# Performance work log

Measured on AMD Instinct MI355X. Metric: run time of the kernel, lower is better.

The kernel has to match this reference:

```python
import jax, jax.numpy as jnp
import numpy as np

LN_EPS = 1e-5


def setup_inputs() -> dict:
    key = jax.random.key(0)
    k1, k2, k3, k4, k5 = jax.random.split(key, 5)
    V, D_REAL, D_HID, D_MODEL = 32000, 768, 512, 4096
    B, S = 4, 2048
    return {
        "real": jax.random.normal(k1, (V, D_REAL), dtype=jnp.float32),
        "llama_embed": jax.random.normal(k2, (V, D_MODEL), dtype=jnp.float32),
        "w1": jax.random.normal(k3, (D_HID, D_REAL), dtype=jnp.float32),  # trans_1.weight
        "w2": jax.random.normal(k4, (D_MODEL, D_HID), dtype=jnp.float32),  # trans_2.weight
        "ln_w": jnp.ones((D_HID,), dtype=jnp.float32),
        "ln_b": jnp.zeros((D_HID,), dtype=jnp.float32),
        "input_ids": jax.random.randint(k5, (B, S), 0, V, dtype=jnp.int64),
    }


def _layernorm(x, w, b):
    mu = jnp.mean(x, axis=-1, keepdims=True)
    var = jnp.mean(jnp.square(x - mu), axis=-1, keepdims=True)
    return (x - mu) * jax.lax.rsqrt(var + LN_EPS) * w + b


def reference(real, llama_embed, w1, w2, ln_w, ln_b, input_ids):
    # trans_2(ELU(LayerNorm(trans_1(real)))) over the FULL table, as in the original
    h = jnp.einsum("vd,hd->vh", real, w1)            # [V, 512]
    h = jax.nn.elu(_layernorm(h, ln_w, ln_b))        # [V, 512]
    transfered = jnp.einsum("vh,mh->vm", h, w2)      # [V, 4096]
    # gather rows per token and add frozen llama embeddings
    return transfered[input_ids] + llama_embed[input_ids]  # [B, S, 4096]
```

## Files before the change

kernel.cpp:

```cpp
#include <hip/hip_runtime.h>
#include <hip/hip_bf16.h>
#include <math.h>

#define TOKENS 8192
#define D_REAL 768
#define D_HID  512
#define D_MODEL 4096

typedef __attribute__((ext_vector_type(8))) short bf16x8;
typedef __attribute__((ext_vector_type(4))) float f32x4;

__device__ inline unsigned short f2bf(float f) {
    union { float f; unsigned u; } v; v.f = f;
    unsigned r = v.u + 0x7FFFu + ((v.u >> 16) & 1u);
    return (unsigned short)(r >> 16);
}
__device__ inline float bf2f(unsigned short h) {
    union { unsigned u; float f; } v; v.u = ((unsigned)h) << 16;
    return v.f;
}

__device__ inline void gload_lds16(const void* g, void* lds_wave_base) {
    __builtin_amdgcn_global_load_lds(
        (const __attribute__((address_space(1))) unsigned*)g,
        (__attribute__((address_space(3))) unsigned*)lds_wave_base,
        16, 0, 0);
}

template<int K, int N, bool ADD_EMBED, bool OUT_BF16>
__global__ __launch_bounds__(256)
void gemm_mfma(const unsigned short* __restrict__ A,
               const unsigned short* __restrict__ B,
               const int* __restrict__ ids,
               const float* __restrict__ embed,
               void* __restrict__ Cout)
{
    __shared__ __align__(16) unsigned short As[128 * 32];
    __shared__ __align__(16) unsigned short Bs[128 * 32];
    __shared__ int sIds[128];

    const int tid = threadIdx.x;
    const int rowBase = blockIdx.x * 128;
    const int colBase = blockIdx.y * 128;

    if (ADD_EMBED && tid < 128) sIds[tid] = ids[rowBase + tid];

    const int srow = tid >> 2;
    const int scol = (tid & 3) * 8;
    const unsigned short* gA = A + (size_t)(rowBase + srow) * K + scol;
    const unsigned short* gB = B + (size_t)(colBase + srow) * K + scol;
    unsigned short* lA = As + (tid >> 6) * 512;
    unsigned short* lB = Bs + (tid >> 6) * 512;

    const int lane = tid & 63;
    const int wv   = tid >> 6;
    const int wm   = (wv >> 1) * 64;
    const int wn   = (wv & 1) * 64;
    const int frow = lane & 15;
    const int fk   = (lane >> 4) * 8;

    f32x4 acc[4][4];
    #pragma unroll
    for (int i = 0; i < 4; i++)
        #pragma unroll
        for (int j = 0; j < 4; j++) acc[i][j] = (f32x4)0.f;

    for (int k0 = 0; k0 < K; k0 += 32) {
        gload_lds16(gA,                lA);
        gload_lds16(gA + (size_t)64*K, lA + 2048);
        gload_lds16(gB,                lB);
        gload_lds16(gB + (size_t)64*K, lB + 2048);
        gA += 32; gB += 32;
        __syncthreads();

        bf16x8 af[4], bg[4];
        #pragma unroll
        for (int i = 0; i < 4; i++)
            af[i] = *reinterpret_cast<const bf16x8*>(&As[(wm + i*16 + frow) * 32 + fk]);
        #pragma unroll
        for (int j = 0; j < 4; j++)
            bg[j] = *reinterpret_cast<const bf16x8*>(&Bs[(wn + j*16 + frow) * 32 + fk]);

        #pragma unroll
        for (int i = 0; i < 4; i++)
            #pragma unroll
            for (int j = 0; j < 4; j++)
                acc[i][j] = __builtin_amdgcn_mfma_f32_16x16x32_bf16(af[i], bg[j], acc[i][j], 0, 0, 0);
        __syncthreads();
    }

    const int orow0 = wm + (lane >> 4) * 4;
    const int ocol0 = wn + frow;
    #pragma unroll
    for (int i = 0; i < 4; i++) {
        #pragma unroll
        for (int r = 0; r < 4; r++) {
            const int lrow = orow0 + i * 16 + r;
            const size_t grow = (size_t)(rowBase + lrow);
            if (OUT_BF16) {
                unsigned short* C = (unsigned short*)Cout;
                #pragma unroll
                for (int j = 0; j < 4; j++)
                    C[grow * N + colBase + ocol0 + j * 16] = f2bf(acc[i][j][r]);
            } else {
                float* C = (float*)Cout;
                const float* e = ADD_EMBED
                    ? embed + (size_t)sIds[lrow] * N + colBase + ocol0 : nullptr;
                #pragma unroll
                for (int j = 0; j < 4; j++) {
                    float v = acc[i][j][r];
                    if (ADD_EMBED) v += e[j * 16];
                    C[grow * N + colBase + ocol0 + j * 16] = v;
                }
            }
        }
    }
}

__global__ __launch_bounds__(256)
void convert_bf16(const float* __restrict__ src, unsigned short* __restrict__ dst, int n4)
{
    const int i = blockIdx.x * 256 + threadIdx.x;
    if (i >= n4) return;
    const float4 v = reinterpret_cast<const float4*>(src)[i];
    ushort4 o;
    o.x = f2bf(v.x); o.y = f2bf(v.y); o.z = f2bf(v.z); o.w = f2bf(v.w);
    reinterpret_cast<ushort4*>(dst)[i] = o;
}

__global__ __launch_bounds__(192)
void gather_bf16(const float* __restrict__ real, const int* __restrict__ ids,
                 unsigned short* __restrict__ Ag)
{
    const int row = blockIdx.x;
    const int t = threadIdx.x;
    const float4 v = *reinterpret_cast<const float4*>(real + (size_t)ids[row] * D_REAL + t * 4);
    ushort4 o;
    o.x = f2bf(v.x); o.y = f2bf(v.y); o.z = f2bf(v.z); o.w = f2bf(v.w);
    *reinterpret_cast<ushort4*>(Ag + (size_t)row * D_REAL + t * 4) = o;
}

__global__ __launch_bounds__(256)
void ln_elu_bf16(unsigned short* __restrict__ H,
                 const float* __restrict__ ln_w, const float* __restrict__ ln_b)
{
    const int row = blockIdx.x * 4 + (threadIdx.x >> 6);
    const int t = threadIdx.x & 63;
    unsigned short* x = H + (size_t)row * D_HID + t * 8;

    bf16x8 v = *reinterpret_cast<const bf16x8*>(x);
    float f[8], s = 0.f, ss = 0.f;
    #pragma unroll
    for (int j = 0; j < 8; j++) {
        f[j] = bf2f((unsigned short)v[j]);
        s += f[j]; ss += f[j] * f[j];
    }
    #pragma unroll
    for (int off = 32; off > 0; off >>= 1) {
        s  += __shfl_down(s, off);
        ss += __shfl_down(ss, off);
    }
    s = __shfl(s, 0); ss = __shfl(ss, 0);
    const float mu = s * (1.f / D_HID);
    const float var = ss * (1.f / D_HID) - mu * mu;
    const float rstd = rsqrtf(var + 1e-5f);

    const float4 w0 = *reinterpret_cast<const float4*>(ln_w + t * 8);
    const float4 w1 = *reinterpret_cast<const float4*>(ln_w + t * 8 + 4);
    const float4 b0 = *reinterpret_cast<const float4*>(ln_b + t * 8);
    const float4 b1 = *reinterpret_cast<const float4*>(ln_b + t * 8 + 4);
    const float wa[8] = { w0.x, w0.y, w0.z, w0.w, w1.x, w1.y, w1.z, w1.w };
    const float ba[8] = { b0.x, b0.y, b0.z, b0.w, b1.x, b1.y, b1.z, b1.w };

    bf16x8 o;
    #pragma unroll
    for (int j = 0; j < 8; j++) {
        float y = (f[j] - mu) * rstd * wa[j] + ba[j];
        y = y > 0.f ? y : expm1f(y);
        o[j] = (short)f2bf(y);
    }
    *reinterpret_cast<bf16x8*>(x) = o;
}

extern "C" void kernel_launch(void* const* d_in, const int* in_sizes, int n_in,
                              void* d_out, int out_size, void* d_ws, size_t ws_size,
                              hipStream_t stream)
{
    const float* real  = (const float*)d_in[0];
    const float* embed = (const float*)d_in[1];
    const float* w1    = (const float*)d_in[2];
    const float* w2    = (const float*)d_in[3];
    const float* ln_w  = (const float*)d_in[4];
    const float* ln_b  = (const float*)d_in[5];
    const int*   ids   = (const int*)d_in[6];
    float* out = (float*)d_out;

    unsigned short* Hb  = (unsigned short*)d_ws;
    unsigned short* w1b = Hb  + (size_t)TOKENS * D_HID;
    unsigned short* w2b = w1b + (size_t)D_HID * D_REAL;
    unsigned short* Ag  = (unsigned short*)d_out;

    convert_bf16<<<(D_HID * D_REAL / 4 + 255) / 256, 256, 0, stream>>>(w1, w1b, D_HID * D_REAL / 4);
    convert_bf16<<<(D_MODEL * D_HID / 4 + 255) / 256, 256, 0, stream>>>(w2, w2b, D_MODEL * D_HID / 4);
    gather_bf16<<<TOKENS, 192, 0, stream>>>(real, ids, Ag);

    dim3 g1(TOKENS / 128, D_HID / 128);
    gemm_mfma<D_REAL, D_HID, false, true><<<g1, 256, 0, stream>>>(Ag, w1b, nullptr, nullptr, Hb);

    ln_elu_bf16<<<TOKENS / 4, 256, 0, stream>>>(Hb, ln_w, ln_b);

    dim3 g2(TOKENS / 128, D_MODEL / 128);
    gemm_mfma<D_HID, D_MODEL, true, false><<<g2, 256, 0, stream>>>(Hb, w2b, ids, embed, out);
}
```

Baseline: 136.3 us.

## Fuse gather, first GEMM, and LayerNorm+ELU into one kernel

Replaces the gather, w1 conversion, first GEMM and separate LayerNorm/ELU kernels with one kernel. Each 1024-thread block computes a full 64x512 hidden tile, converts fp32 inputs to bf16 on the fly while staging into LDS, and applies LayerNorm and ELU in registers using a cross-wave reduction. This removes three launches and the bf16 round-trips of the gathered inputs and the hidden activations through global memory. In exchange, the first GEMM runs on only 128 blocks, uses synchronous register-staged loads, and re-reads and re-converts w1 in every block.

```diff
diff --git a/kernel.cpp b/kernel.cpp
--- a/kernel.cpp
+++ b/kernel.cpp
@@ -15,9 +15,16 @@
     unsigned r = v.u + 0x7FFFu + ((v.u >> 16) & 1u);
     return (unsigned short)(r >> 16);
 }
-__device__ inline float bf2f(unsigned short h) {
-    union { unsigned u; float f; } v; v.u = ((unsigned)h) << 16;
-    return v.f;
+__device__ inline unsigned pack2(float lo, float hi) {
+    return (unsigned)f2bf(lo) | ((unsigned)f2bf(hi) << 16);
+}
+__device__ inline bf16x8 cvt8(float4 a, float4 b) {
+    bf16x8 r;
+    r[0] = (short)f2bf(a.x); r[1] = (short)f2bf(a.y);
+    r[2] = (short)f2bf(a.z); r[3] = (short)f2bf(a.w);
+    r[4] = (short)f2bf(b.x); r[5] = (short)f2bf(b.y);
+    r[6] = (short)f2bf(b.z); r[7] = (short)f2bf(b.w);
+    return r;
 }
 
 __device__ inline void gload_lds16(const void* g, void* lds_wave_base) {
@@ -27,14 +34,132 @@
         16, 0, 0);
 }
 
-template<int K, int N, bool ADD_EMBED, bool OUT_BF16>
+__global__ __launch_bounds__(1024)
+void gemm1_ln(const float* __restrict__ real, const float* __restrict__ w1,
+              const int* __restrict__ ids,
+              const float* __restrict__ ln_w, const float* __restrict__ ln_b,
+              unsigned short* __restrict__ H)
+{
+    __shared__ __align__(16) unsigned short As[64 * 32];
+    __shared__ __align__(16) unsigned short Bs[512 * 32];
+    __shared__ float redS[64][8];
+    __shared__ float redQ[64][8];
+    __shared__ int sIds[64];
+
+    const int tid = threadIdx.x;
+    const int rowBase = blockIdx.x * 64;
+    if (tid < 64) sIds[tid] = ids[rowBase + tid];
+    __syncthreads();
+
+    const int ar = tid >> 4;
+    const int ac = (tid & 15) * 2;
+    const int br = tid >> 1;
+    const int bh = (tid & 1) * 16;
+
+    const float* gA = real + (size_t)sIds[ar] * D_REAL + ac;
+    const float* gB = w1 + (size_t)br * D_REAL + bh;
+
+    const int lane = tid & 63;
+    const int wv = tid >> 6;
+    const int wr = wv >> 3;
+    const int wc = wv & 7;
+    const int frow = lane & 15;
+    const int fk = (lane >> 4) * 8;
+
+    f32x4 acc[2][4];
+    #pragma unroll
+    for (int i = 0; i < 2; i++)
+        #pragma unroll
+        for (int j = 0; j < 4; j++) acc[i][j] = (f32x4)0.f;
+
+    for (int k0 = 0; k0 < D_REAL; k0 += 32) {
+        const float2 av = *reinterpret_cast<const float2*>(gA + k0);
+        const float4 b0 = *reinterpret_cast<const float4*>(gB + k0);
+        const float4 b1 = *reinterpret_cast<const float4*>(gB + k0 + 4);
+        const float4 b2 = *reinterpret_cast<const float4*>(gB + k0 + 8);
+        const float4 b3 = *reinterpret_cast<const float4*>(gB + k0 + 12);
+        __syncthreads();
+        reinterpret_cast<unsigned*>(As)[ar * 16 + (ac >> 1)] = pack2(av.x, av.y);
+        *reinterpret_cast<bf16x8*>(&Bs[br * 32 + bh])     = cvt8(b0, b1);
+        *reinterpret_cast<bf16x8*>(&Bs[br * 32 + bh + 8]) = cvt8(b2, b3);
+        __syncthreads();
+
+        bf16x8 af[2], bg[4];
+        #pragma unroll
+        for (int i = 0; i < 2; i++)
+            af[i] = *reinterpret_cast<const bf16x8*>(&As[(wr*32 + i*16 + frow) * 32 + fk]);
+        #pragma unroll
+        for (int j = 0; j < 4; j++)
+            bg[j] = *reinterpret_cast<const bf16x8*>(&Bs[(wc*64 + j*16 + frow) * 32 + fk]);
+        #pragma unroll
+        for (int i = 0; i < 2; i++)
+            #pragma unroll
+            for (int j = 0; j < 4; j++)
+                acc[i][j] = __builtin_amdgcn_mfma_f32_16x16x32_bf16(af[i], bg[j], acc[i][j], 0, 0, 0);
+    }
+    __syncthreads();
+
+    #pragma unroll
+    for (int i = 0; i < 2; i++) {
+        #pragma unroll
+        for (int r = 0; r < 4; r++) {
+            float s = 0.f, q = 0.f;
+            #pragma unroll
+            for (int j = 0; j < 4; j++) {
+                const float v = acc[i][j][r];
+                s += v; q += v * v;
+            }
+            #pragma unroll
+            for (int m = 1; m < 16; m <<= 1) {
+                s += __shfl_xor(s, m);
+                q += __shfl_xor(q, m);
+            }
+            if (frow == 0) {
+                const int row = wr*32 + i*16 + (lane >> 4)*4 + r;
+                redS[row][wc] = s;
+                redQ[row][wc] = q;
+            }
+        }
+    }
+    __syncthreads();
+
+    float wcol[4], bcol[4];
+    #pragma unroll
+    for (int j = 0; j < 4; j++) {
+        const int col = wc*64 + j*16 + frow;
+        wcol[j] = ln_w[col];
+        bcol[j] = ln_b[col];
+    }
+    #pragma unroll
+    for (int i = 0; i < 2; i++) {
+        #pragma unroll
+        for (int r = 0; r < 4; r++) {
+            const int row = wr*32 + i*16 + (lane >> 4)*4 + r;
+            float sum = 0.f, sq = 0.f;
+            #pragma unroll
+            for (int w = 0; w < 8; w++) { sum += redS[row][w]; sq += redQ[row][w]; }
+            const float mu = sum * (1.f / D_HID);
+            const float var = sq * (1.f / D_HID) - mu * mu;
+            const float rstd = rsqrtf(var + 1e-5f);
+            unsigned short* dst = H + (size_t)(rowBase + row) * D_HID + wc*64 + frow;
+            #pragma unroll
+            for (int j = 0; j < 4; j++) {
+                float y = (acc[i][j][r] - mu) * rstd * wcol[j] + bcol[j];
+                y = y > 0.f ? y : expm1f(y);
+                dst[j * 16] = f2bf(y);
+            }
+        }
+    }
+}
+
 __global__ __launch_bounds__(256)
-void gemm_mfma(const unsigned short* __restrict__ A,
-               const unsigned short* __restrict__ B,
-               const int* __restrict__ ids,
-               const float* __restrict__ embed,
-               void* __restrict__ Cout)
-{
+void gemm2_mfma(const unsigned short* __restrict__ A,
+                const unsigned short* __restrict__ B,
+                const int* __restrict__ ids,
+                const float* __restrict__ embed,
+                float* __restrict__ C)
+{
+    constexpr int K = D_HID, N = D_MODEL;
     __shared__ __align__(16) unsigned short As[128 * 32];
     __shared__ __align__(16) unsigned short Bs[128 * 32];
     __shared__ int sIds[128];
@@ -43,7 +168,7 @@
     const int rowBase = blockIdx.x * 128;
     const int colBase = blockIdx.y * 128;
 
-    if (ADD_EMBED && tid < 128) sIds[tid] = ids[rowBase + tid];
+    if (tid < 128) sIds[tid] = ids[rowBase + tid];
 
     const int srow = tid >> 2;
     const int scol = (tid & 3) * 8;
@@ -97,22 +222,10 @@
         for (int r = 0; r < 4; r++) {
             const int lrow = orow0 + i * 16 + r;
             const size_t grow = (size_t)(rowBase + lrow);
-            if (OUT_BF16) {
-                unsigned short* C = (unsigned short*)Cout;
-                #pragma unroll
-                for (int j = 0; j < 4; j++)
-                    C[grow * N + colBase + ocol0 + j * 16] = f2bf(acc[i][j][r]);
-            } else {
-                float* C = (float*)Cout;
-                const float* e = ADD_EMBED
-                    ? embed + (size_t)sIds[lrow] * N + colBase + ocol0 : nullptr;
-                #pragma unroll
-                for (int j = 0; j < 4; j++) {
-                    float v = acc[i][j][r];
-                    if (ADD_EMBED) v += e[j * 16];
-                    C[grow * N + colBase + ocol0 + j * 16] = v;
-                }
-            }
+            const float* e = embed + (size_t)sIds[lrow] * N + colBase + ocol0;
+            #pragma unroll
+            for (int j = 0; j < 4; j++)
+                C[grow * N + colBase + ocol0 + j * 16] = acc[i][j][r] + e[j * 16];
         }
     }
 }
@@ -126,60 +239,6 @@
     ushort4 o;
     o.x = f2bf(v.x); o.y = f2bf(v.y); o.z = f2bf(v.z); o.w = f2bf(v.w);
     reinterpret_cast<ushort4*>(dst)[i] = o;
-}
-
-__global__ __launch_bounds__(192)
-void gather_bf16(const float* __restrict__ real, const int* __restrict__ ids,
-                 unsigned short* __restrict__ Ag)
-{
-    const int row = blockIdx.x;
-    const int t = threadIdx.x;
-    const float4 v = *reinterpret_cast<const float4*>(real + (size_t)ids[row] * D_REAL + t * 4);
-    ushort4 o;
-    o.x = f2bf(v.x); o.y = f2bf(v.y); o.z = f2bf(v.z); o.w = f2bf(v.w);
-    *reinterpret_cast<ushort4*>(Ag + (size_t)row * D_REAL + t * 4) = o;
-}
-
-__global__ __launch_bounds__(256)
-void ln_elu_bf16(unsigned short* __restrict__ H,
-                 const float* __restrict__ ln_w, const float* __restrict__ ln_b)
-{
-    const int row = blockIdx.x * 4 + (threadIdx.x >> 6);
-    const int t = threadIdx.x & 63;
-    unsigned short* x = H + (size_t)row * D_HID + t * 8;
-
-    bf16x8 v = *reinterpret_cast<const bf16x8*>(x);
-    float f[8], s = 0.f, ss = 0.f;
-    #pragma unroll
-    for (int j = 0; j < 8; j++) {
-        f[j] = bf2f((unsigned short)v[j]);
-        s += f[j]; ss += f[j] * f[j];
-    }
-    #pragma unroll
-    for (int off = 32; off > 0; off >>= 1) {
-        s  += __shfl_down(s, off);
-        ss += __shfl_down(ss, off);
-    }
-    s = __shfl(s, 0); ss = __shfl(ss, 0);
-    const float mu = s * (1.f / D_HID);
-    const float var = ss * (1.f / D_HID) - mu * mu;
-    const float rstd = rsqrtf(var + 1e-5f);
-
-    const float4 w0 = *reinterpret_cast<const float4*>(ln_w + t * 8);
-    const float4 w1 = *reinterpret_cast<const float4*>(ln_w + t * 8 + 4);
-    const float4 b0 = *reinterpret_cast<const float4*>(ln_b + t * 8);
-    const float4 b1 = *reinterpret_cast<const float4*>(ln_b + t * 8 + 4);
-    const float wa[8] = { w0.x, w0.y, w0.z, w0.w, w1.x, w1.y, w1.z, w1.w };
-    const float ba[8] = { b0.x, b0.y, b0.z, b0.w, b1.x, b1.y, b1.z, b1.w };
-
-    bf16x8 o;
-    #pragma unroll
-    for (int j = 0; j < 8; j++) {
-        float y = (f[j] - mu) * rstd * wa[j] + ba[j];
-        y = y > 0.f ? y : expm1f(y);
-        o[j] = (short)f2bf(y);
-    }
-    *reinterpret_cast<bf16x8*>(x) = o;
 }
 
 extern "C" void kernel_launch(void* const* d_in, const int* in_sizes, int n_in,
@@ -196,19 +255,12 @@
     float* out = (float*)d_out;
 
     unsigned short* Hb  = (unsigned short*)d_ws;
-    unsigned short* w1b = Hb  + (size_t)TOKENS * D_HID;
-    unsigned short* w2b = w1b + (size_t)D_HID * D_REAL;
-    unsigned short* Ag  = (unsigned short*)d_out;
-
-    convert_bf16<<<(D_HID * D_REAL / 4 + 255) / 256, 256, 0, stream>>>(w1, w1b, D_HID * D_REAL / 4);
+    unsigned short* w2b = Hb + (size_t)TOKENS * D_HID;
+
     convert_bf16<<<(D_MODEL * D_HID / 4 + 255) / 256, 256, 0, stream>>>(w2, w2b, D_MODEL * D_HID / 4);
-    gather_bf16<<<TOKENS, 192, 0, stream>>>(real, ids, Ag);
-
-    dim3 g1(TOKENS / 128, D_HID / 128);
-    gemm_mfma<D_REAL, D_HID, false, true><<<g1, 256, 0, stream>>>(Ag, w1b, nullptr, nullptr, Hb);
-
-    ln_elu_bf16<<<TOKENS / 4, 256, 0, stream>>>(Hb, ln_w, ln_b);
+
+    gemm1_ln<<<TOKENS / 64, 1024, 0, stream>>>(real, w1, ids, ln_w, ln_b, Hb);
 
     dim3 g2(TOKENS / 128, D_MODEL / 128);
-    gemm_mfma<D_HID, D_MODEL, true, false><<<g2, 256, 0, stream>>>(Hb, w2b, ids, embed, out);
-}
+    gemm2_mfma<<<g2, 256, 0, stream>>>(Hb, w2b, ids, embed, out);
+}
```

After: 176.1 us. 29.2% more time.
